# Kernel optimization log

Measured on AMD Instinct MI355X. Metric: run time of the kernel, lower is better.

Reference implementation:

```python
import jax, jax.numpy as jnp
import numpy as np

B, C, N = 2, 64, 40000
MLP = [64, 64, 128]
EPS = 1e-5


def setup_inputs() -> dict:
    key = jax.random.key(0)
    ks = jax.random.split(key, 2 + 4 * len(MLP))
    inp = {
        "points": jax.random.normal(ks[0], (B, C, N), dtype=jnp.float32),
        "near_idx": jax.random.randint(ks[1], (N, 6), 0, 2 * N, dtype=jnp.int32),
    }
    last = 2 * C
    for i, out_ch in enumerate(MLP):
        k = 2 + 4 * i
        scale = 1.0 / np.sqrt(last)
        inp[f"W{i}"] = jax.random.normal(ks[k], (out_ch, last), dtype=jnp.float32) * scale
        inp[f"b{i}"] = jax.random.normal(ks[k + 1], (out_ch,), dtype=jnp.float32) * 0.01
        inp[f"g{i}"] = jnp.ones((out_ch,), dtype=jnp.float32)
        inp[f"beta{i}"] = jnp.zeros((out_ch,), dtype=jnp.float32)
        last = out_ch
    return inp


def _mlp_bn_relu(x, W, b, g, beta):
    # x: [B, N, 6, Cin]; 1x1 conv == channel matmul
    y = jnp.einsum("bnkc,oc->bnko", x, W) + b
    mu = y.mean(axis=(0, 1, 2))
    var = y.var(axis=(0, 1, 2))  # biased, matches BN training normalization
    y = (y - mu) * jax.lax.rsqrt(var + EPS) * g + beta
    return jax.nn.relu(y)


def reference(points, near_idx, W0, b0, g0, beta0, W1, b1, g1, beta1, W2, b2, g2, beta2):
    x = jnp.transpose(points, (0, 2, 1))          # [B, N, C]
    pad = jnp.full_like(x, -1.0)                  # out-of-index block (-1 fill)
    xpad = jnp.concatenate([x, pad], axis=1)      # [B, 2N, C]
    near = xpad[:, near_idx, :]                   # [B, N, 6, C] irregular gather
    feat = jnp.concatenate(
        [jnp.broadcast_to(x[:, :, None, :], near.shape), near], axis=3
    )                                             # [B, N, 6, 2C]
    feat = _mlp_bn_relu(feat, W0, b0, g0, beta0)
    feat = _mlp_bn_relu(feat, W1, b1, g1, beta1)
    feat = _mlp_bn_relu(feat, W2, b2, g2, beta2)  # [B, N, 6, C']
    new_feature = feat.max(axis=2)                # max over 6 neighbors -> [B, N, C']
    new_feature = jnp.transpose(new_feature, (0, 2, 1))  # [B, C', N] (torch layout)
    out_feature = new_feature.max(axis=1)         # max over channels -> [B, N]
    return (out_feature, new_feature)
```

## Files before the change

kernel.cpp:

```cpp
#include <hip/hip_runtime.h>

typedef unsigned short u16;
typedef unsigned int uint;
typedef short bf16x8 __attribute__((ext_vector_type(8)));
typedef float f32x4 __attribute__((ext_vector_type(4)));

constexpr int B_ = 2;
constexpr int N_ = 40000;
constexpr int SPB = 240000;
constexpr int S_ = B_ * SPB;
constexpr float EPS_ = 1e-5f;
constexpr float INV_S = 1.0f / (float)S_;
constexpr int OF_ = B_ * N_;
constexpr int TILES_PB = SPB / 48;

constexpr int      WS_V_U16   = B_ * N_ * 128;
constexpr size_t   NEED_BIG_B = 81955072ull;

__device__ inline float b2f_lo(uint u) { return __builtin_bit_cast(float, u << 16); }
__device__ inline float b2f_hi(uint u) { return __builtin_bit_cast(float, u & 0xffff0000u); }
__device__ inline u16 f2b(float f) {
    uint b = __builtin_bit_cast(uint, f);
    return (u16)((b + 0x7fffu + ((b >> 16) & 1u)) >> 16);
}
__device__ inline void unp8(uint4 q, float* f) {
    f[0] = b2f_lo(q.x); f[1] = b2f_hi(q.x); f[2] = b2f_lo(q.y); f[3] = b2f_hi(q.y);
    f[4] = b2f_lo(q.z); f[5] = b2f_hi(q.z); f[6] = b2f_lo(q.w); f[7] = b2f_hi(q.w);
}

__global__ __launch_bounds__(256) void wprep_kernel(const float* __restrict__ W0,
                                                    const float* __restrict__ W1,
                                                    const float* __restrict__ W2,
                                                    float* __restrict__ stats,
                                                    float* __restrict__ neg2,
                                                    u16* __restrict__ pack) {
    const int t = threadIdx.x;
    stats[t] = 0.f; stats[t + 256] = 0.f;
    if (t < 64) {
        float s = 0.f;
        for (int j = 0; j < 64; ++j) s += W0[t * 128 + 64 + j];
        neg2[t] = -s;
    }
    for (int g = t; g < 40 * 64; g += 256) {
        int lane = g & 63, grp = g >> 6;
        int cb = lane & 15, kq = lane >> 4;
        ushort4 lo, hi;
        u16* dst;
        if (grp < 16) {
            int ct = grp >> 1, kk = grp & 1;
            int c = ct * 16 + cb, jb = kk * 32 + kq * 8;
            dst = pack + g * 8;
            float v[8];
            #pragma unroll
            for (int i = 0; i < 8; ++i)
                v[i] = (c < 64) ? W0[c * 128 + jb + i] : W0[(c - 64) * 128 + 64 + jb + i];
            lo = {f2b(v[0]), f2b(v[1]), f2b(v[2]), f2b(v[3])};
            hi = {f2b(v[4]), f2b(v[5]), f2b(v[6]), f2b(v[7])};
        } else if (grp < 24) {
            int g2 = grp - 16;
            int ct = g2 >> 1, kk = g2 & 1;
            const float* wp = W1 + (ct * 16 + cb) * 64 + kk * 32 + kq * 8;
            dst = pack + 8192 + (g2 * 64 + lane) * 8;
            lo = {f2b(wp[0]), f2b(wp[1]), f2b(wp[2]), f2b(wp[3])};
            hi = {f2b(wp[4]), f2b(wp[5]), f2b(wp[6]), f2b(wp[7])};
        } else {
            int g3 = grp - 24;
            int ct = g3 >> 1, kk = g3 & 1;
            const float* wp = W2 + (ct * 16 + cb) * 64 + kk * 32 + kq * 8;
            dst = pack + 12288 + (g3 * 64 + lane) * 8;
            lo = {f2b(wp[0]), f2b(wp[1]), f2b(wp[2]), f2b(wp[3])};
            hi = {f2b(wp[4]), f2b(wp[5]), f2b(wp[6]), f2b(wp[7])};
        }
        *(ushort4*)dst = lo;
        *(ushort4*)(dst + 4) = hi;
    }
}

__global__ __launch_bounds__(256) void p0_kernel(const float* __restrict__ pts,
                                                 const u16* __restrict__ pack,
                                                 u16* __restrict__ V) {
    const int t = threadIdx.x, lane = t & 63, w = t >> 6;
    const int cb = lane & 15, kq = lane >> 4;
    const int b = blockIdx.y;
    const int n0 = blockIdx.x * 192 + w * 48;
    const uint4* mp = (const uint4*)pack;

    bf16x8 af[3][2];
    #pragma unroll
    for (int mt = 0; mt < 3; ++mt) {
        int n = n0 + mt * 16 + cb;
        int nc = (n < N_) ? n : (N_ - 1);
        const float* xp = pts + b * 64 * N_ + nc;
        #pragma unroll
        for (int kk = 0; kk < 2; ++kk) {
            int jb = kk * 32 + kq * 8;
            #pragma unroll
            for (int i = 0; i < 8; ++i)
                af[mt][kk][i] = (short)f2b(xp[(size_t)(jb + i) * N_]);
        }
    }
    #pragma unroll
    for (int ct = 0; ct < 8; ++ct) {
        bf16x8 b0 = __builtin_bit_cast(bf16x8, mp[(ct * 2 + 0) * 64 + lane]);
        bf16x8 b1 = __builtin_bit_cast(bf16x8, mp[(ct * 2 + 1) * 64 + lane]);
        #pragma unroll
        for (int mt = 0; mt < 3; ++mt) {
            f32x4 acc = {};
            acc = __builtin_amdgcn_mfma_f32_16x16x32_bf16(af[mt][0], b0, acc, 0, 0, 0);
            acc = __builtin_amdgcn_mfma_f32_16x16x32_bf16(af[mt][1], b1, acc, 0, 0, 0);
            int rbase = n0 + mt * 16 + kq * 4;
            #pragma unroll
            for (int r = 0; r < 4; ++r) {
                int n = rbase + r;
                if (n < N_) V[(size_t)(b * N_ + n) * 128 + ct * 16 + cb] = f2b(acc[r]);
            }
        }
    }
}

__global__ __launch_bounds__(256) void p1_kernel(const u16* __restrict__ V,
                                                 const int* __restrict__ nidx,
                                                 const float* __restrict__ neg2,
                                                 float* __restrict__ stats) {
    const int t = threadIdx.x, lane = t & 63, w = t >> 6;
    const int slot = lane >> 3, cg = lane & 7;
    const int b = blockIdx.y;
    const int s0 = blockIdx.x * 384 + w * 96;
    float ngs8[8];
    #pragma unroll
    for (int i = 0; i < 8; ++i) ngs8[i] = neg2[cg * 8 + i];
    float sum[8] = {0,0,0,0,0,0,0,0}, sq[8] = {0,0,0,0,0,0,0,0};
    #pragma unroll 4
    for (int it = 0; it < 12; ++it) {
        int s = s0 + it * 8 + slot;
        int n = s / 6;
        int m = nidx[s];
        bool valid = (m < N_);
        int row2 = valid ? (b * N_ + m) : 0;
        uint4 q1 = *(const uint4*)(V + (size_t)(b * N_ + n) * 128 + cg * 8);
        uint4 q2 = *(const uint4*)(V + (size_t)row2 * 128 + 64 + cg * 8);
        float v1[8], v2[8];
        unp8(q1, v1); unp8(q2, v2);
        #pragma unroll
        for (int i = 0; i < 8; ++i) {
            float z = v1[i] + (valid ? v2[i] : ngs8[i]);
            sum[i] += z; sq[i] = fmaf(z, z, sq[i]);
        }
    }
    #pragma unroll
    for (int i = 0; i < 8; ++i) {
        sum[i] += __shfl_xor(sum[i], 8); sum[i] += __shfl_xor(sum[i], 16); sum[i] += __shfl_xor(sum[i], 32);
        sq[i]  += __shfl_xor(sq[i], 8);  sq[i]  += __shfl_xor(sq[i], 16);  sq[i]  += __shfl_xor(sq[i], 32);
    }
    __shared__ float red[2][4][64];
    if (slot == 0) {
        #pragma unroll
        for (int i = 0; i < 8; ++i) { red[0][w][cg * 8 + i] = sum[i]; red[1][w][cg * 8 + i] = sq[i]; }
    }
    __syncthreads();
    if (t < 64) {
        float s_ = (red[0][0][t] + red[0][1][t]) + (red[0][2][t] + red[0][3][t]);
        float q_ = (red[1][0][t] + red[1][1][t]) + (red[1][2][t] + red[1][3][t]);
        atomicAdd(&stats[t], s_);
        atomicAdd(&stats[64 + t], q_);
    }
}

__device__ inline bf16x8 build_af(const u16* __restrict__ V, int row1, int row2,
                                  const float* adt0, const float* adt1,
                                  const float* ngs, int j0) {
    float v1f[8], v2f[8];
    uint4 q1 = *(const uint4*)(V + (size_t)row1 * 128 + j0);
    unp8(q1, v1f);
    if (row2 >= 0) {
        uint4 q2 = *(const uint4*)(V + (size_t)row2 * 128 + 64 + j0);
        unp8(q2, v2f);
    } else {
        #pragma unroll
        for (int i = 0; i < 8; ++i) v2f[i] = ngs[j0 + i];
    }
    bf16x8 r;
    #pragma unroll
    for (int i = 0; i < 8; ++i) {
        float f0 = fmaxf((v1f[i] + v2f[i]) * adt0[j0 + i] + adt1[j0 + i], 0.f);
        r[i] = (short)f2b(f0);
    }
    return r;
}

__device__ inline int sigma_sl(int mt, int cb) {
    int r_ = cb & 3, kqr = cb >> 2;
    int idx = mt * 4 + r_;
    int po = (idx >= 6) ? 1 : 0;
    return (kqr * 2 + po) * 6 + (idx - 6 * po);
}

template<int STOREZ1>
__global__ __launch_bounds__(256) void p2_kernel(const u16* __restrict__ V,
                                                 const int* __restrict__ nidx,
                                                 const float* __restrict__ neg2,
                                                 const u16* __restrict__ pack,
                                                 const float* __restrict__ g0,
                                                 const float* __restrict__ beta0,
                                                 float* __restrict__ stats,
                                                 u16* __restrict__ z1buf) {
    __shared__ float adt0[64], adt1[64], ngs[64];
    __shared__ float red[2][4][64];
    const int t = threadIdx.x, lane = t & 63, w = t >> 6;
    const int cb = lane & 15, kq = lane >> 4;
    if (t < 64) {
        float mu = stats[t] * INV_S, vr = stats[64 + t] * INV_S - mu * mu;
        float a = rsqrtf(vr + EPS_) * g0[t];
        adt0[t] = a; adt1[t] = beta0[t] - mu * a; ngs[t] = neg2[t];
    }
    __syncthreads();
    const int b = blockIdx.y;
    const int slb = blockIdx.x * 192 + w * 48;
    const uint4* w1p = (const uint4*)(pack + 8192);
    uint2* ztile = STOREZ1 ? ((uint2*)z1buf + ((size_t)b * TILES_PB + blockIdx.x * 4 + w) * (12 * 64)) : nullptr;

    bf16x8 bf[4][2];
    #pragma unroll
    for (int ct = 0; ct < 4; ++ct)
        #pragma unroll
        for (int kk = 0; kk < 2; ++kk)
            bf[ct][kk] = __builtin_bit_cast(bf16x8, w1p[(ct * 2 + kk) * 64 + lane]);

    float ssum[4] = {0,0,0,0}, ssq[4] = {0,0,0,0};
    #pragma unroll
    for (int mt = 0; mt < 3; ++mt) {
        int sl = slb + sigma_sl(mt, cb);
        int n = sl / 6;
        int m = nidx[sl];
        int row1 = b * N_ + n;
        int row2 = (m < N_) ? (b * N_ + m) : -1;
        bf16x8 af[2];
        #pragma unroll
        for (int kk = 0; kk < 2; ++kk)
            af[kk] = build_af(V, row1, row2, adt0, adt1, ngs, kk * 32 + kq * 8);
        f32x4 acc[4] = {};
        #pragma unroll
        for (int ct = 0; ct < 4; ++ct) {
            acc[ct] = __builtin_amdgcn_mfma_f32_16x16x32_bf16(af[0], bf[ct][0], acc[ct], 0, 0, 0);
            acc[ct] = __builtin_amdgcn_mfma_f32_16x16x32_bf16(af[1], bf[ct][1], acc[ct], 0, 0, 0);
        }
        #pragma unroll
        for (int ct = 0; ct < 4; ++ct) {
            #pragma unroll
            for (int r = 0; r < 4; ++r) {
                float z = acc[ct][r];
                ssum[ct] += z; ssq[ct] = fmaf(z, z, ssq[ct]);
            }
            if constexpr (STOREZ1) {
                uint lo = (uint)f2b(acc[ct][0]) | ((uint)f2b(acc[ct][1]) << 16);
                uint hi = (uint)f2b(acc[ct][2]) | ((uint)f2b(acc[ct][3]) << 16);
                ztile[(mt * 4 + ct) * 64 + lane] = {lo, hi};
            }
        }
    }
    #pragma unroll
    for (int ct = 0; ct < 4; ++ct) {
        ssum[ct] += __shfl_xor(ssum[ct], 16); ssum[ct] += __shfl_xor(ssum[ct], 32);
        ssq[ct]  += __shfl_xor(ssq[ct], 16);  ssq[ct]  += __shfl_xor(ssq[ct], 32);
    }
    if (lane < 16) {
        #pragma unroll
        for (int ct = 0; ct < 4; ++ct) {
            red[0][w][ct * 16 + lane] = ssum[ct];
            red[1][w][ct * 16 + lane] = ssq[ct];
        }
    }
    __syncthreads();
    if (t < 64) {
        float s = (red[0][0][t] + red[0][1][t]) + (red[0][2][t] + red[0][3][t]);
        float q = (red[1][0][t] + red[1][1][t]) + (red[1][2][t] + red[1][3][t]);
        atomicAdd(&stats[128 + t], s);
        atomicAdd(&stats[192 + t], q);
    }
}

template<int LOADZ1>
__global__ __launch_bounds__(256) void p3_kernel(const u16* __restrict__ V,
                                                 const int* __restrict__ nidx,
                                                 const float* __restrict__ neg2,
                                                 const u16* __restrict__ pack,
                                                 const float* __restrict__ g0, const float* __restrict__ beta0,
                                                 const float* __restrict__ g1, const float* __restrict__ beta1,
                                                 const float* __restrict__ g2,
                                                 float* __restrict__ stats,
                                                 const u16* __restrict__ z1buf,
                                                 float* __restrict__ out) {
    __shared__ u16   f1t[4][16 * 64];
    __shared__ float smax[32][129];
    __shared__ float red[2][4][128];
    __shared__ float adt2s[64], adt3s[64], psign[128];
    __shared__ float adt0s[64], adt1s[64], ngs[64];
    const int t = threadIdx.x, lane = t & 63, w = t >> 6;
    const int cb = lane & 15, kq = lane >> 4;
    if (t < 64) {
        float mu1 = stats[128 + t] * INV_S, vr1 = stats[192 + t] * INV_S - mu1 * mu1;
        float a1 = rsqrtf(vr1 + EPS_) * g1[t];
        adt2s[t] = a1; adt3s[t] = beta1[t] - mu1 * a1;
        if constexpr (!LOADZ1) {
            float mu0 = stats[t] * INV_S, vr0 = stats[64 + t] * INV_S - mu0 * mu0;
            float a0 = rsqrtf(vr0 + EPS_) * g0[t];
            adt0s[t] = a0; adt1s[t] = beta0[t] - mu0 * a0; ngs[t] = neg2[t];
        }
    }
    if (t < 128) psign[t] = (g2[t] >= 0.f) ? 1.f : -1.f;
    __syncthreads();

    const int b = blockIdx.y;
    const int slb = blockIdx.x * 192 + w * 48;
    const uint4* w1p = (const uint4*)(pack + 8192);
    const uint4* w2p = (const uint4*)(pack + 12288);
    const uint2* zt = LOADZ1 ? ((const uint2*)z1buf + ((size_t)b * TILES_PB + blockIdx.x * 4 + w) * (12 * 64)) : nullptr;

    bf16x8 bf2[8][2];
    #pragma unroll
    for (int u = 0; u < 8; ++u)
        #pragma unroll
        for (int kk = 0; kk < 2; ++kk)
            bf2[u][kk] = __builtin_bit_cast(bf16x8, w2p[(u * 2 + kk) * 64 + lane]);

    float a1c[4], d1c[4];
    #pragma unroll
    for (int ct = 0; ct < 4; ++ct) { a1c[ct] = adt2s[ct * 16 + cb]; d1c[ct] = adt3s[ct * 16 + cb]; }

    float pmax_[2][4][2];
    #pragma unroll
    for (int h = 0; h < 2; ++h)
        #pragma unroll
        for (int ct = 0; ct < 4; ++ct) { pmax_[h][ct][0] = -3.402823466e+38f; pmax_[h][ct][1] = -3.402823466e+38f; }
    float ssum[8] = {0,0,0,0,0,0,0,0}, ssq[8] = {0,0,0,0,0,0,0,0};
    u16* fb = f1t[w];

    #pragma unroll
    for (int mt = 0; mt < 3; ++mt) {
        f32x4 z1v[4];
        if constexpr (LOADZ1) {
            #pragma unroll
            for (int ct = 0; ct < 4; ++ct) {
                uint2 q = zt[(mt * 4 + ct) * 64 + lane];
                z1v[ct][0] = b2f_lo(q.x); z1v[ct][1] = b2f_hi(q.x);
                z1v[ct][2] = b2f_lo(q.y); z1v[ct][3] = b2f_hi(q.y);
            }
        } else {
            bf16x8 bf1[4][2];
            #pragma unroll
            for (int ct = 0; ct < 4; ++ct)
                #pragma unroll
                for (int kk = 0; kk < 2; ++kk)
                    bf1[ct][kk] = __builtin_bit_cast(bf16x8, w1p[(ct * 2 + kk) * 64 + lane]);
            int sl = slb + sigma_sl(mt, cb);
            int n = sl / 6;
            int m = nidx[sl];
            int row1 = b * N_ + n;
            int row2 = (m < N_) ? (b * N_ + m) : -1;
            bf16x8 af[2];
            #pragma unroll
            for (int kk = 0; kk < 2; ++kk)
                af[kk] = build_af(V, row1, row2, adt0s, adt1s, ngs, kk * 32 + kq * 8);
            #pragma unroll
            for (int ct = 0; ct < 4; ++ct) {
                f32x4 a = {};
                a = __builtin_amdgcn_mfma_f32_16x16x32_bf16(af[0], bf1[ct][0], a, 0, 0, 0);
                a = __builtin_amdgcn_mfma_f32_16x16x32_bf16(af[1], bf1[ct][1], a, 0, 0, 0);
                z1v[ct] = a;
            }
        }
        #pragma unroll
        for (int ct = 0; ct < 4; ++ct) {
            #pragma unroll
            for (int r = 0; r < 4; ++r) {
                float f1 = fmaxf(z1v[ct][r] * a1c[ct] + d1c[ct], 0.f);
                int rw = kq * 4 + r;
                fb[rw * 64 + ((ct * 16 + cb) ^ ((rw & 7) << 3))] = f2b(f1);
            }
        }
        bf16x8 af2[2];
        #pragma unroll
        for (int kk = 0; kk < 2; ++kk) {
            int j0 = kk * 32 + kq * 8;
            af2[kk] = __builtin_bit_cast(bf16x8, *(const uint4*)(fb + cb * 64 + (j0 ^ ((cb & 7) << 3))));
        }
        #pragma unroll
        for (int half = 0; half < 2; ++half) {
            f32x4 acc2[4] = {};
            #pragma unroll
            for (int ct = 0; ct < 4; ++ct) {
                acc2[ct] = __builtin_amdgcn_mfma_f32_16x16x32_bf16(af2[0], bf2[half * 4 + ct][0], acc2[ct], 0, 0, 0);
                acc2[ct] = __builtin_amdgcn_mfma_f32_16x16x32_bf16(af2[1], bf2[half * 4 + ct][1], acc2[ct], 0, 0, 0);
            }
            #pragma unroll
            for (int ct = 0; ct < 4; ++ct) {
                float ps = psign[half * 64 + ct * 16 + cb];
                #pragma unroll
                for (int r = 0; r < 4; ++r) {
                    float z = acc2[ct][r];
                    ssum[half * 4 + ct] += z;
                    ssq[half * 4 + ct] = fmaf(z, z, ssq[half * 4 + ct]);
                    float zz = z * ps;
                    int pi = (mt == 0) ? 0 : ((mt == 2) ? 1 : ((r >= 2) ? 1 : 0));
                    pmax_[half][ct][pi] = fmaxf(pmax_[half][ct][pi], zz);
                }
            }
        }
    }
    #pragma unroll
    for (int half = 0; half < 2; ++half)
        #pragma unroll
        for (int ct = 0; ct < 4; ++ct)
            #pragma unroll
            for (int p = 0; p < 2; ++p)
                smax[w * 8 + kq * 2 + p][half * 64 + ct * 16 + cb] = pmax_[half][ct][p];
    #pragma unroll
    for (int j = 0; j < 8; ++j) {
        ssum[j] += __shfl_xor(ssum[j], 16); ssum[j] += __shfl_xor(ssum[j], 32);
        ssq[j]  += __shfl_xor(ssq[j], 16);  ssq[j]  += __shfl_xor(ssq[j], 32);
    }
    if (lane < 16) {
        #pragma unroll
        for (int j = 0; j < 8; ++j) {
            int c = (j >> 2) * 64 + (j & 3) * 16 + lane;
            red[0][w][c] = ssum[j];
            red[1][w][c] = ssq[j];
        }
    }
    __syncthreads();
    if (t < 128) {
        float s = (red[0][0][t] + red[0][1][t]) + (red[0][2][t] + red[0][3][t]);
        float q = (red[1][0][t] + red[1][1][t]) + (red[1][2][t] + red[1][3][t]);
        atomicAdd(&stats[256 + t], s);
        atomicAdd(&stats[384 + t], q);
    }
    {
        int c2 = t >> 1, nh = t & 1;
        float ps = psign[c2];
        float* op = out + OF_ + ((size_t)b * 128 + c2) * N_ + blockIdx.x * 32 + nh * 16;
        #pragma unroll
        for (int i4 = 0; i4 < 4; ++i4) {
            float4 v;
            v.x = smax[nh * 16 + i4 * 4 + 0][c2] * ps;
            v.y = smax[nh * 16 + i4 * 4 + 1][c2] * ps;
            v.z = smax[nh * 16 + i4 * 4 + 2][c2] * ps;
            v.w = smax[nh * 16 + i4 * 4 + 3][c2] * ps;
            *(float4*)(op + i4 * 4) = v;
        }
    }
}

__global__ __launch_bounds__(256) void p4_kernel(const float* __restrict__ g2,
                                                 const float* __restrict__ beta2,
                                                 const float* __restrict__ stats,
                                                 float* __restrict__ outbuf) {
    __shared__ float a2s[128], d2s[128];
    const int t = threadIdx.x;
    if (t < 128) {
        float mu = stats[256 + t] * INV_S;
        float vr = stats[384 + t] * INV_S - mu * mu;
        float a = rsqrtf(vr + EPS_) * g2[t];
        a2s[t] = a;
        d2s[t] = beta2[t] - mu * a;
    }
    __syncthreads();
    const int b = blockIdx.y;
    const int n = blockIdx.x * 256 + t;
    if (n >= N_) return;
    float vmax = -3.402823466e+38f;
    #pragma unroll 8
    for (int c2 = 0; c2 < 128; ++c2) {
        size_t idx = OF_ + ((size_t)b * 128 + c2) * N_ + n;
        float v = fmaxf(outbuf[idx] * a2s[c2] + d2s[c2], 0.f);
        outbuf[idx] = v;
        vmax = fmaxf(vmax, v);
    }
    outbuf[b * N_ + n] = vmax;
}

extern "C" void kernel_launch(void* const* d_in, const int* in_sizes, int n_in,
                              void* d_out, int out_size, void* d_ws, size_t ws_size,
                              hipStream_t stream) {
    (void)in_sizes; (void)n_in; (void)out_size;
    const float* pts   = (const float*)d_in[0];
    const int*   nidx  = (const int*)d_in[1];
    const float* W0    = (const float*)d_in[2];
    const float* g0    = (const float*)d_in[4];
    const float* beta0 = (const float*)d_in[5];
    const float* W1    = (const float*)d_in[6];
    const float* g1    = (const float*)d_in[8];
    const float* beta1 = (const float*)d_in[9];
    const float* W2    = (const float*)d_in[10];
    const float* g2    = (const float*)d_in[12];
    const float* beta2 = (const float*)d_in[13];
    const bool big = ws_size >= NEED_BIG_B;
    u16*   V     = (u16*)d_ws;
    u16*   z1b   = big ? ((u16*)d_ws + WS_V_U16) : nullptr;
    float* stats = (float*)d_ws + (big ? 20480000 : 5120000);
    float* neg2  = stats + 512;
    u16*   pack  = (u16*)d_ws + (big ? 40961152 : 10241152);
    float* out   = (float*)d_out;

    hipLaunchKernelGGL(wprep_kernel, dim3(1), dim3(256), 0, stream, W0, W1, W2, stats, neg2, pack);
    hipLaunchKernelGGL(p0_kernel, dim3((N_ + 191) / 192, B_), dim3(256), 0, stream, pts, pack, V);
    hipLaunchKernelGGL(p1_kernel, dim3(SPB / 384, B_), dim3(256), 0, stream, V, nidx, neg2, stats);
    if (big) {
        hipLaunchKernelGGL((p2_kernel<1>), dim3(SPB / 192, B_), dim3(256), 0, stream,
                           V, nidx, neg2, pack, g0, beta0, stats, z1b);
        hipLaunchKernelGGL((p3_kernel<1>), dim3(SPB / 192, B_), dim3(256), 0, stream,
                           V, nidx, neg2, pack, g0, beta0, g1, beta1, g2, stats, z1b, out);
    } else {
        hipLaunchKernelGGL((p2_kernel<0>), dim3(SPB / 192, B_), dim3(256), 0, stream,
                           V, nidx, neg2, pack, g0, beta0, stats, z1b);
        hipLaunchKernelGGL((p3_kernel<0>), dim3(SPB / 192, B_), dim3(256), 0, stream,
                           V, nidx, neg2, pack, g0, beta0, g1, beta1, g2, stats, z1b, out);
    }
    hipLaunchKernelGGL(p4_kernel, dim3((N_ + 255) / 256, B_), dim3(256), 0, stream, g2, beta2, stats, out);
}
```

Measured before the change: 309.1 us.

## Split p3/p4 into big-workspace variants storing bf16 raw maxima and batching gathers

Adds a dedicated p3big kernel that reads the stored z1 tiles with 16-byte loads and double-buffers the shared-memory BN1 tile across the three row-tiles. It writes the pre-BN2 per-point maxima as bf16 into the reused V buffer instead of fp32 into the output. A new p4big kernel reads those bf16 values, applies BN2 and ReLU, writes the fp32 output, and reduces the channel max across four channel groups per block. p1 and p2 now issue their index and gather loads in batches to raise memory-level parallelism, and p2 writes z1 as uint4. The intent is less global traffic and better latency hiding, at the cost of bf16 rounding of the pre-BN maxima and more register pressure.

```diff
diff --git a/kernel.cpp b/kernel.cpp
--- a/kernel.cpp
+++ b/kernel.cpp
@@ -19,10 +19,12 @@
 
 __device__ inline float b2f_lo(uint u) { return __builtin_bit_cast(float, u << 16); }
 __device__ inline float b2f_hi(uint u) { return __builtin_bit_cast(float, u & 0xffff0000u); }
+__device__ inline float b2fu(u16 s)    { return __builtin_bit_cast(float, ((uint)s) << 16); }
 __device__ inline u16 f2b(float f) {
     uint b = __builtin_bit_cast(uint, f);
     return (u16)((b + 0x7fffu + ((b >> 16) & 1u)) >> 16);
 }
+__device__ inline uint pk2(float a, float b) { return (uint)f2b(a) | ((uint)f2b(b) << 16); }
 __device__ inline void unp8(uint4 q, float* f) {
     f[0] = b2f_lo(q.x); f[1] = b2f_hi(q.x); f[2] = b2f_lo(q.y); f[3] = b2f_hi(q.y);
     f[4] = b2f_lo(q.z); f[5] = b2f_hi(q.z); f[6] = b2f_lo(q.w); f[7] = b2f_hi(q.w);
@@ -130,21 +132,30 @@
     #pragma unroll
     for (int i = 0; i < 8; ++i) ngs8[i] = neg2[cg * 8 + i];
     float sum[8] = {0,0,0,0,0,0,0,0}, sq[8] = {0,0,0,0,0,0,0,0};
-    #pragma unroll 4
-    for (int it = 0; it < 12; ++it) {
-        int s = s0 + it * 8 + slot;
-        int n = s / 6;
-        int m = nidx[s];
-        bool valid = (m < N_);
-        int row2 = valid ? (b * N_ + m) : 0;
-        uint4 q1 = *(const uint4*)(V + (size_t)(b * N_ + n) * 128 + cg * 8);
-        uint4 q2 = *(const uint4*)(V + (size_t)row2 * 128 + 64 + cg * 8);
-        float v1[8], v2[8];
-        unp8(q1, v1); unp8(q2, v2);
-        #pragma unroll
-        for (int i = 0; i < 8; ++i) {
-            float z = v1[i] + (valid ? v2[i] : ngs8[i]);
-            sum[i] += z; sq[i] = fmaf(z, z, sq[i]);
+    #pragma unroll
+    for (int h = 0; h < 2; ++h) {
+        int mh[6]; uint4 q1[6], q2[6]; bool val[6];
+        #pragma unroll
+        for (int it = 0; it < 6; ++it) {
+            int s = s0 + (h * 6 + it) * 8 + slot;
+            mh[it] = nidx[s];
+            q1[it] = *(const uint4*)(V + (size_t)(b * N_ + s / 6) * 128 + cg * 8);
+        }
+        #pragma unroll
+        for (int it = 0; it < 6; ++it) {
+            val[it] = (mh[it] < N_);
+            int row2 = val[it] ? (b * N_ + mh[it]) : 0;
+            q2[it] = *(const uint4*)(V + (size_t)row2 * 128 + 64 + cg * 8);
+        }
+        #pragma unroll
+        for (int it = 0; it < 6; ++it) {
+            float v1[8], v2[8];
+            unp8(q1[it], v1); unp8(q2[it], v2);
+            #pragma unroll
+            for (int i = 0; i < 8; ++i) {
+                float z = v1[i] + (val[it] ? v2[i] : ngs8[i]);
+                sum[i] += z; sq[i] = fmaf(z, z, sq[i]);
+            }
         }
     }
     #pragma unroll
@@ -188,8 +199,8 @@
     return r;
 }
 
-__device__ inline int sigma_sl(int mt, int cb) {
-    int r_ = cb & 3, kqr = cb >> 2;
+__device__ inline int sigma_sl(int mt, int row) {
+    int r_ = row & 3, kqr = row >> 2;
     int idx = mt * 4 + r_;
     int po = (idx >= 6) ? 1 : 0;
     return (kqr * 2 + po) * 6 + (idx - 6 * po);
@@ -217,7 +228,11 @@
     const int b = blockIdx.y;
     const int slb = blockIdx.x * 192 + w * 48;
     const uint4* w1p = (const uint4*)(pack + 8192);
-    uint2* ztile = STOREZ1 ? ((uint2*)z1buf + ((size_t)b * TILES_PB + blockIdx.x * 4 + w) * (12 * 64)) : nullptr;
+    uint4* zt4 = STOREZ1 ? ((uint4*)z1buf + ((size_t)b * TILES_PB + blockIdx.x * 4 + w) * (6 * 64)) : nullptr;
+
+    int m_[3];
+    #pragma unroll
+    for (int mt = 0; mt < 3; ++mt) m_[mt] = nidx[slb + sigma_sl(mt, cb)];
 
     bf16x8 bf[4][2];
     #pragma unroll
@@ -231,9 +246,8 @@
     for (int mt = 0; mt < 3; ++mt) {
         int sl = slb + sigma_sl(mt, cb);
         int n = sl / 6;
-        int m = nidx[sl];
         int row1 = b * N_ + n;
-        int row2 = (m < N_) ? (b * N_ + m) : -1;
+        int row2 = (m_[mt] < N_) ? (b * N_ + m_[mt]) : -1;
         bf16x8 af[2];
         #pragma unroll
         for (int kk = 0; kk < 2; ++kk)
@@ -245,16 +259,21 @@
             acc[ct] = __builtin_amdgcn_mfma_f32_16x16x32_bf16(af[1], bf[ct][1], acc[ct], 0, 0, 0);
         }
         #pragma unroll
-        for (int ct = 0; ct < 4; ++ct) {
+        for (int ct = 0; ct < 4; ++ct)
             #pragma unroll
             for (int r = 0; r < 4; ++r) {
                 float z = acc[ct][r];
                 ssum[ct] += z; ssq[ct] = fmaf(z, z, ssq[ct]);
             }
-            if constexpr (STOREZ1) {
-                uint lo = (uint)f2b(acc[ct][0]) | ((uint)f2b(acc[ct][1]) << 16);
-                uint hi = (uint)f2b(acc[ct][2]) | ((uint)f2b(acc[ct][3]) << 16);
-                ztile[(mt * 4 + ct) * 64 + lane] = {lo, hi};
+        if constexpr (STOREZ1) {
+            #pragma unroll
+            for (int cp = 0; cp < 2; ++cp) {
+                uint4 o;
+                o.x = pk2(acc[cp * 2][0], acc[cp * 2][1]);
+                o.y = pk2(acc[cp * 2][2], acc[cp * 2][3]);
+                o.z = pk2(acc[cp * 2 + 1][0], acc[cp * 2 + 1][1]);
+                o.w = pk2(acc[cp * 2 + 1][2], acc[cp * 2 + 1][3]);
+                zt4[(mt * 2 + cp) * 64 + lane] = o;
             }
         }
     }
@@ -279,17 +298,163 @@
     }
 }
 
-template<int LOADZ1>
-__global__ __launch_bounds__(256) void p3_kernel(const u16* __restrict__ V,
-                                                 const int* __restrict__ nidx,
-                                                 const float* __restrict__ neg2,
-                                                 const u16* __restrict__ pack,
-                                                 const float* __restrict__ g0, const float* __restrict__ beta0,
-                                                 const float* __restrict__ g1, const float* __restrict__ beta1,
-                                                 const float* __restrict__ g2,
-                                                 float* __restrict__ stats,
-                                                 const u16* __restrict__ z1buf,
-                                                 float* __restrict__ out) {
+__global__ __launch_bounds__(256) void p3big_kernel(const u16* __restrict__ z1buf,
+                                                    const u16* __restrict__ pack,
+                                                    const float* __restrict__ g1, const float* __restrict__ beta1,
+                                                    const float* __restrict__ g2,
+                                                    float* __restrict__ stats,
+                                                    u16* __restrict__ raw) {
+    __shared__ u16   f1t[4][2][1024];
+    __shared__ float smax[32][129];
+    __shared__ float red[2][4][128];
+    __shared__ float adt2s[64], adt3s[64], psign[128];
+    const int t = threadIdx.x, lane = t & 63, w = t >> 6;
+    const int cb = lane & 15, kq = lane >> 4;
+    if (t < 64) {
+        float mu1 = stats[128 + t] * INV_S, vr1 = stats[192 + t] * INV_S - mu1 * mu1;
+        float a1 = rsqrtf(vr1 + EPS_) * g1[t];
+        adt2s[t] = a1; adt3s[t] = beta1[t] - mu1 * a1;
+    }
+    if (t < 128) psign[t] = (g2[t] >= 0.f) ? 1.f : -1.f;
+    __syncthreads();
+
+    const int b = blockIdx.y;
+    const uint4* zt4 = (const uint4*)z1buf + ((size_t)b * TILES_PB + blockIdx.x * 4 + w) * (6 * 64);
+    const uint4* w2p = (const uint4*)(pack + 12288);
+
+    uint4 zq[6];
+    #pragma unroll
+    for (int i = 0; i < 6; ++i) zq[i] = zt4[i * 64 + lane];
+
+    bf16x8 bf2[8][2];
+    #pragma unroll
+    for (int u = 0; u < 8; ++u)
+        #pragma unroll
+        for (int kk = 0; kk < 2; ++kk)
+            bf2[u][kk] = __builtin_bit_cast(bf16x8, w2p[(u * 2 + kk) * 64 + lane]);
+
+    float a1c[4], d1c[4];
+    #pragma unroll
+    for (int ct = 0; ct < 4; ++ct) { a1c[ct] = adt2s[ct * 16 + cb]; d1c[ct] = adt3s[ct * 16 + cb]; }
+
+    float pmax_[2][4][2];
+    #pragma unroll
+    for (int h = 0; h < 2; ++h)
+        #pragma unroll
+        for (int ct = 0; ct < 4; ++ct) { pmax_[h][ct][0] = -3.402823466e+38f; pmax_[h][ct][1] = -3.402823466e+38f; }
+    float ssum[8] = {0,0,0,0,0,0,0,0}, ssq[8] = {0,0,0,0,0,0,0,0};
+    u16* fb0 = f1t[w][0];
+    u16* fb1 = f1t[w][1];
+
+    auto BNW = [&](int mt, u16* fb) {
+        #pragma unroll
+        for (int cp = 0; cp < 2; ++cp) {
+            uint4 q = zq[mt * 2 + cp];
+            float za[4] = {b2f_lo(q.x), b2f_hi(q.x), b2f_lo(q.y), b2f_hi(q.y)};
+            float zb[4] = {b2f_lo(q.z), b2f_hi(q.z), b2f_lo(q.w), b2f_hi(q.w)};
+            int ca = cp * 2, cc = cp * 2 + 1;
+            #pragma unroll
+            for (int r = 0; r < 4; ++r) {
+                int rw = kq * 4 + r;
+                fb[rw * 64 + ((ca * 16 + cb) ^ ((rw & 7) << 3))] = f2b(fmaxf(za[r] * a1c[ca] + d1c[ca], 0.f));
+                fb[rw * 64 + ((cc * 16 + cb) ^ ((rw & 7) << 3))] = f2b(fmaxf(zb[r] * a1c[cc] + d1c[cc], 0.f));
+            }
+        }
+    };
+    auto RDA = [&](const u16* fb, bf16x8* af2) {
+        #pragma unroll
+        for (int kk = 0; kk < 2; ++kk) {
+            int j0 = kk * 32 + kq * 8;
+            af2[kk] = __builtin_bit_cast(bf16x8, *(const uint4*)(fb + cb * 64 + (j0 ^ ((cb & 7) << 3))));
+        }
+    };
+    auto MM = [&](int mt, const bf16x8* af2) {
+        #pragma unroll
+        for (int half = 0; half < 2; ++half) {
+            f32x4 acc2[4] = {};
+            #pragma unroll
+            for (int ct = 0; ct < 4; ++ct) {
+                acc2[ct] = __builtin_amdgcn_mfma_f32_16x16x32_bf16(af2[0], bf2[half * 4 + ct][0], acc2[ct], 0, 0, 0);
+                acc2[ct] = __builtin_amdgcn_mfma_f32_16x16x32_bf16(af2[1], bf2[half * 4 + ct][1], acc2[ct], 0, 0, 0);
+            }
+            #pragma unroll
+            for (int ct = 0; ct < 4; ++ct) {
+                float ps = psign[half * 64 + ct * 16 + cb];
+                #pragma unroll
+                for (int r = 0; r < 4; ++r) {
+                    float z = acc2[ct][r];
+                    ssum[half * 4 + ct] += z;
+                    ssq[half * 4 + ct] = fmaf(z, z, ssq[half * 4 + ct]);
+                    float zz = z * ps;
+                    int pi = (mt == 0) ? 0 : ((mt == 2) ? 1 : ((r >= 2) ? 1 : 0));
+                    pmax_[half][ct][pi] = fmaxf(pmax_[half][ct][pi], zz);
+                }
+            }
+        }
+    };
+
+    bf16x8 afA[2], afB[2];
+    BNW(0, fb0); BNW(1, fb1);
+    RDA(fb0, afA);
+    MM(0, afA);
+    BNW(2, fb0);
+    RDA(fb1, afB);
+    MM(1, afB);
+    RDA(fb0, afA);
+    MM(2, afA);
+
+    #pragma unroll
+    for (int half = 0; half < 2; ++half)
+        #pragma unroll
+        for (int ct = 0; ct < 4; ++ct)
+            #pragma unroll
+            for (int p = 0; p < 2; ++p)
+                smax[w * 8 + kq * 2 + p][half * 64 + ct * 16 + cb] = pmax_[half][ct][p];
+    #pragma unroll
+    for (int j = 0; j < 8; ++j) {
+        ssum[j] += __shfl_xor(ssum[j], 16); ssum[j] += __shfl_xor(ssum[j], 32);
+        ssq[j]  += __shfl_xor(ssq[j], 16);  ssq[j]  += __shfl_xor(ssq[j], 32);
+    }
+    if (lane < 16) {
+        #pragma unroll
+        for (int j = 0; j < 8; ++j) {
+            int c = (j >> 2) * 64 + (j & 3) * 16 + lane;
+            red[0][w][c] = ssum[j];
+            red[1][w][c] = ssq[j];
+        }
+    }
+    __syncthreads();
+    if (t < 128) {
+        float s = (red[0][0][t] + red[0][1][t]) + (red[0][2][t] + red[0][3][t]);
+        float q = (red[1][0][t] + red[1][1][t]) + (red[1][2][t] + red[1][3][t]);
+        atomicAdd(&stats[256 + t], s);
+        atomicAdd(&stats[384 + t], q);
+    }
+    {
+        int c2 = t >> 1, nh = t & 1;
+        float ps = psign[c2];
+        u16* rp = raw + ((size_t)b * 128 + c2) * N_ + blockIdx.x * 32 + nh * 16;
+        #pragma unroll
+        for (int i4 = 0; i4 < 4; ++i4) {
+            ushort4 v;
+            v.x = f2b(smax[nh * 16 + i4 * 4 + 0][c2] * ps);
+            v.y = f2b(smax[nh * 16 + i4 * 4 + 1][c2] * ps);
+            v.z = f2b(smax[nh * 16 + i4 * 4 + 2][c2] * ps);
+            v.w = f2b(smax[nh * 16 + i4 * 4 + 3][c2] * ps);
+            *(ushort4*)(rp + i4 * 4) = v;
+        }
+    }
+}
+
+__global__ __launch_bounds__(256) void p3small_kernel(const u16* __restrict__ V,
+                                                      const int* __restrict__ nidx,
+                                                      const float* __restrict__ neg2,
+                                                      const u16* __restrict__ pack,
+                                                      const float* __restrict__ g0, const float* __restrict__ beta0,
+                                                      const float* __restrict__ g1, const float* __restrict__ beta1,
+                                                      const float* __restrict__ g2,
+                                                      float* __restrict__ stats,
+                                                      float* __restrict__ out) {
     __shared__ u16   f1t[4][16 * 64];
     __shared__ float smax[32][129];
     __shared__ float red[2][4][128];
@@ -301,11 +466,9 @@
         float mu1 = stats[128 + t] * INV_S, vr1 = stats[192 + t] * INV_S - mu1 * mu1;
         float a1 = rsqrtf(vr1 + EPS_) * g1[t];
         adt2s[t] = a1; adt3s[t] = beta1[t] - mu1 * a1;
-        if constexpr (!LOADZ1) {
-            float mu0 = stats[t] * INV_S, vr0 = stats[64 + t] * INV_S - mu0 * mu0;
-            float a0 = rsqrtf(vr0 + EPS_) * g0[t];
-            adt0s[t] = a0; adt1s[t] = beta0[t] - mu0 * a0; ngs[t] = neg2[t];
-        }
+        float mu0 = stats[t] * INV_S, vr0 = stats[64 + t] * INV_S - mu0 * mu0;
+        float a0 = rsqrtf(vr0 + EPS_) * g0[t];
+        adt0s[t] = a0; adt1s[t] = beta0[t] - mu0 * a0; ngs[t] = neg2[t];
     }
     if (t < 128) psign[t] = (g2[t] >= 0.f) ? 1.f : -1.f;
     __syncthreads();
@@ -314,7 +477,6 @@
     const int slb = blockIdx.x * 192 + w * 48;
     const uint4* w1p = (const uint4*)(pack + 8192);
     const uint4* w2p = (const uint4*)(pack + 12288);
-    const uint2* zt = LOADZ1 ? ((const uint2*)z1buf + ((size_t)b * TILES_PB + blockIdx.x * 4 + w) * (12 * 64)) : nullptr;
 
     bf16x8 bf2[8][2];
     #pragma unroll
@@ -337,47 +499,37 @@
 
     #pragma unroll
     for (int mt = 0; mt < 3; ++mt) {
+        bf16x8 bf1[4][2];
+        #pragma unroll
+        for (int ct = 0; ct < 4; ++ct)
+            #pragma unroll
+            for (int kk = 0; kk < 2; ++kk)
+                bf1[ct][kk] = __builtin_bit_cast(bf16x8, w1p[(ct * 2 + kk) * 64 + lane]);
+        int sl = slb + sigma_sl(mt, cb);
+        int n = sl / 6;
+        int m = nidx[sl];
+        int row1 = b * N_ + n;
+        int row2 = (m < N_) ? (b * N_ + m) : -1;
+        bf16x8 af[2];
+        #pragma unroll
+        for (int kk = 0; kk < 2; ++kk)
+            af[kk] = build_af(V, row1, row2, adt0s, adt1s, ngs, kk * 32 + kq * 8);
         f32x4 z1v[4];
-        if constexpr (LOADZ1) {
-            #pragma unroll
-            for (int ct = 0; ct < 4; ++ct) {
-                uint2 q = zt[(mt * 4 + ct) * 64 + lane];
-                z1v[ct][0] = b2f_lo(q.x); z1v[ct][1] = b2f_hi(q.x);
-                z1v[ct][2] = b2f_lo(q.y); z1v[ct][3] = b2f_hi(q.y);
-            }
-        } else {
-            bf16x8 bf1[4][2];
-            #pragma unroll
-            for (int ct = 0; ct < 4; ++ct)
-                #pragma unroll
-                for (int kk = 0; kk < 2; ++kk)
-                    bf1[ct][kk] = __builtin_bit_cast(bf16x8, w1p[(ct * 2 + kk) * 64 + lane]);
-            int sl = slb + sigma_sl(mt, cb);
-            int n = sl / 6;
-            int m = nidx[sl];
-            int row1 = b * N_ + n;
-            int row2 = (m < N_) ? (b * N_ + m) : -1;
-            bf16x8 af[2];
-            #pragma unroll
-            for (int kk = 0; kk < 2; ++kk)
-                af[kk] = build_af(V, row1, row2, adt0s, adt1s, ngs, kk * 32 + kq * 8);
-            #pragma unroll
-            for (int ct = 0; ct < 4; ++ct) {
-                f32x4 a = {};
-                a = __builtin_amdgcn_mfma_f32_16x16x32_bf16(af[0], bf1[ct][0], a, 0, 0, 0);
-                a = __builtin_amdgcn_mfma_f32_16x16x32_bf16(af[1], bf1[ct][1], a, 0, 0, 0);
-                z1v[ct] = a;
-            }
-        }
         #pragma unroll
         for (int ct = 0; ct < 4; ++ct) {
+            f32x4 a = {};
+            a = __builtin_amdgcn_mfma_f32_16x16x32_bf16(af[0], bf1[ct][0], a, 0, 0, 0);
+            a = __builtin_amdgcn_mfma_f32_16x16x32_bf16(af[1], bf1[ct][1], a, 0, 0, 0);
+            z1v[ct] = a;
+        }
+        #pragma unroll
+        for (int ct = 0; ct < 4; ++ct)
             #pragma unroll
             for (int r = 0; r < 4; ++r) {
                 float f1 = fmaxf(z1v[ct][r] * a1c[ct] + d1c[ct], 0.f);
                 int rw = kq * 4 + r;
                 fb[rw * 64 + ((ct * 16 + cb) ^ ((rw & 7) << 3))] = f2b(f1);
             }
-        }
         bf16x8 af2[2];
         #pragma unroll
         for (int kk = 0; kk < 2; ++kk) {
@@ -450,10 +602,45 @@
     }
 }
 
-__global__ __launch_bounds__(256) void p4_kernel(const float* __restrict__ g2,
-                                                 const float* __restrict__ beta2,
-                                                 const float* __restrict__ stats,
-                                                 float* __restrict__ outbuf) {
+__global__ __launch_bounds__(256) void p4big_kernel(const float* __restrict__ g2,
+                                                    const float* __restrict__ beta2,
+                                                    const float* __restrict__ stats,
+                                                    const u16* __restrict__ raw,
+                                                    float* __restrict__ out) {
+    __shared__ float a2s[128], d2s[128];
+    __shared__ float vred[4][64];
+    const int t = threadIdx.x, lane = t & 63, cg = t >> 6;
+    if (t < 128) {
+        float mu = stats[256 + t] * INV_S;
+        float vr = stats[384 + t] * INV_S - mu * mu;
+        float a = rsqrtf(vr + EPS_) * g2[t];
+        a2s[t] = a;
+        d2s[t] = beta2[t] - mu * a;
+    }
+    __syncthreads();
+    const int b = blockIdx.y;
+    const int n = blockIdx.x * 64 + lane;
+    const u16* rp = raw + ((size_t)b * 128 + cg * 32) * N_ + n;
+    float* op = out + OF_ + ((size_t)b * 128 + cg * 32) * N_ + n;
+    float vmax = -3.402823466e+38f;
+    #pragma unroll 8
+    for (int c = 0; c < 32; ++c) {
+        int c2 = cg * 32 + c;
+        float v = fmaxf(b2fu(rp[(size_t)c * N_]) * a2s[c2] + d2s[c2], 0.f);
+        op[(size_t)c * N_] = v;
+        vmax = fmaxf(vmax, v);
+    }
+    vred[cg][lane] = vmax;
+    __syncthreads();
+    if (t < 64)
+        out[b * N_ + blockIdx.x * 64 + t] =
+            fmaxf(fmaxf(vred[0][t], vred[1][t]), fmaxf(vred[2][t], vred[3][t]));
+}
+
+__global__ __launch_bounds__(256) void p4small_kernel(const float* __restrict__ g2,
+                                                      const float* __restrict__ beta2,
+                                                      const float* __restrict__ stats,
+                                                      float* __restrict__ outbuf) {
     __shared__ float a2s[128], d2s[128];
     const int t = threadIdx.x;
     if (t < 128) {
@@ -507,13 +694,16 @@
     if (big) {
         hipLaunchKernelGGL((p2_kernel<1>), dim3(SPB / 192, B_), dim3(256), 0, stream,
                            V, nidx, neg2, pack, g0, beta0, stats, z1b);
-        hipLaunchKernelGGL((p3_kernel<1>), dim3(SPB / 192, B_), dim3(256), 0, stream,
-                           V, nidx, neg2, pack, g0, beta0, g1, beta1, g2, stats, z1b, out);
+        hipLaunchKernelGGL(p3big_kernel, dim3(TILES_PB / 4, B_), dim3(256), 0, stream,
+                           z1b, pack, g1, beta1, g2, stats, V);
+        hipLaunchKernelGGL(p4big_kernel, dim3(N_ / 64, B_), dim3(256), 0, stream,
+                           g2, beta2, stats, V, out);
     } else {
         hipLaunchKernelGGL((p2_kernel<0>), dim3(SPB / 192, B_), dim3(256), 0, stream,
-                           V, nidx, neg2, pack, g0, beta0, stats, z1b);
-        hipLaunchKernelGGL((p3_kernel<0>), dim3(SPB / 192, B_), dim3(256), 0, stream,
-                           V, nidx, neg2, pack, g0, beta0, g1, beta1, g2, stats, z1b, out);
-    }
-    hipLaunchKernelGGL(p4_kernel, dim3((N_ + 255) / 256, B_), dim3(256), 0, stream, g2, beta2, stats, out);
-}
+                           V, nidx, neg2, pack, g0, beta0, stats, nullptr);
+        hipLaunchKernelGGL(p3small_kernel, dim3(SPB / 192, B_), dim3(256), 0, stream,
+                           V, nidx, neg2, pack, g0, beta0, g1, beta1, g2, stats, out);
+        hipLaunchKernelGGL(p4small_kernel, dim3((N_ + 255) / 256, B_), dim3(256), 0, stream,
+                           g2, beta2, stats, out);
+    }
+}
```

After: 298.5 us. -3.4%, faster.
